# Kernel tuning notes

Hardware: AMD Instinct MI355X
Metric: run time of the kernel (lower is better)

Reference implementation:

```python
import jax, jax.numpy as jnp
import numpy as np

B, NQ, NKV = 8, 256, 1024
DQ, DK, DV = 256, 256, 256
H = 128  # num_hiddens
NEG_INF = -1e20


def setup_inputs() -> dict:
    key = jax.random.key(0)
    k1, k2, k3, k4, k5, k6, k7 = jax.random.split(key, 7)
    s = 0.05
    return {
        "Q_batch": jax.random.normal(k1, (B, NQ, DQ), jnp.float32),
        "K_batch": jax.random.normal(k2, (B, NKV, DK), jnp.float32),
        "V_batch": jax.random.normal(k3, (B, NKV, DV), jnp.float32),
        "valid_lens": jax.random.randint(k4, (B,), 1, NKV, jnp.int32),
        # Learned params (torch nn.Linear stores weight as (out, in); no bias)
        "Wq": jax.random.normal(k5, (H, DQ), jnp.float32) * s,
        "Wk": jax.random.normal(k6, (H, DK), jnp.float32) * s,
        "Wv": jax.random.normal(k7, (H,), jnp.float32) * s,  # W_v: Linear(H -> 1)
    }


def reference(Q_batch, K_batch, V_batch, valid_lens, Wq, Wk, Wv):
    # Project queries and keys to hidden size H
    q = jnp.einsum('bqd,hd->bqh', Q_batch, Wq)            # (B, NQ, H)
    k = jnp.einsum('bkd,hd->bkh', K_batch, Wk)            # (B, NKV, H)
    # Broadcast add -> tanh -> score projection (materializes (B,NQ,NKV,H))
    S = jnp.tanh(q[:, :, None, :] + k[:, None, :, :])     # (B, NQ, NKV, H)
    scores = jnp.einsum('bqkh,h->bqk', S, Wv)             # (B, NQ, NKV)
    # Masked softmax: 'left' => positions >= valid_len are invalid
    kv_idx = jnp.arange(NKV)                              # (NKV,)
    mask = kv_idx[None, None, :] >= valid_lens[:, None, None]  # (B,1,NKV) broadcast over queries
    scores = jnp.where(mask, NEG_INF, scores)
    attn = jax.nn.softmax(scores, axis=-1)                # (B, NQ, NKV)
    # Dropout is identity in eval mode (rate 0.0)
    return jnp.einsum('bqk,bkv->bqv', attn, V_batch)      # (B, NQ, DV)
```

## Files before the change

kernel.cpp:

```cpp
#include <hip/hip_runtime.h>
#include <hip/hip_bf16.h>
#include <math.h>

#define BB   8
#define NQ   256
#define NKV  1024
#define DD   256
#define HH   128
#define KSPLIT 4
#define KCH  256
#define NITEMS (BB * (NQ / 8) * KSPLIT)
#define NWORK  512

typedef float f16v __attribute__((ext_vector_type(16)));

__global__ __launch_bounds__(256) void proj_exp_kernel(
    const float* __restrict__ Q, const float* __restrict__ K,
    const float* __restrict__ Wq, const float* __restrict__ Wk,
    float* __restrict__ eqb, float* __restrict__ ekb)
{
    __shared__ __align__(16) float At[32][20];
    __shared__ __align__(16) float Wt[32][132];

    const int bid = blockIdx.x;
    const bool isQ = bid < (BB * NQ / 16);
    const float* A = isQ ? Q : K;
    const float* W = isQ ? Wq : Wk;
    float* Out     = isQ ? eqb : ekb;
    const int arow0 = (isQ ? bid : bid - (BB * NQ / 16)) * 16;

    const int tid = threadIdx.x;
    const int rc  = tid >> 5;
    const int hc  = tid & 31;

    float4 c0 = {0.f,0.f,0.f,0.f}, c1 = c0;

    float4 a4;
    float4 w4[4];

    if (tid < 128)
        a4 = *(const float4*)(A + (size_t)(arow0 + (tid >> 3)) * DD + (tid & 7) * 4);
#pragma unroll
    for (int t = 0; t < 4; ++t) {
        int idx = tid + t * 256;
        int h = idx >> 3, dw = idx & 7;
        w4[t] = *(const float4*)(W + (size_t)h * DD + dw * 4);
    }

    for (int ch = 0; ch < 8; ++ch) {
        __syncthreads();
        if (tid < 128) {
            int r_st = tid >> 3, dq = tid & 7;
            At[dq*4+0][r_st] = a4.x;
            At[dq*4+1][r_st] = a4.y;
            At[dq*4+2][r_st] = a4.z;
            At[dq*4+3][r_st] = a4.w;
        }
#pragma unroll
        for (int t = 0; t < 4; ++t) {
            int idx = tid + t * 256;
            int h = idx >> 3, dw = idx & 7;
            Wt[dw*4+0][h] = w4[t].x;
            Wt[dw*4+1][h] = w4[t].y;
            Wt[dw*4+2][h] = w4[t].z;
            Wt[dw*4+3][h] = w4[t].w;
        }
        __syncthreads();
        if (ch + 1 < 8) {
            const int dc = (ch + 1) * 32;
            if (tid < 128)
                a4 = *(const float4*)(A + (size_t)(arow0 + (tid >> 3)) * DD + dc + (tid & 7) * 4);
#pragma unroll
            for (int t = 0; t < 4; ++t) {
                int idx = tid + t * 256;
                int h = idx >> 3, dw = idx & 7;
                w4[t] = *(const float4*)(W + (size_t)h * DD + dc + dw * 4);
            }
        }
#pragma unroll
        for (int d = 0; d < 32; ++d) {
            float a0  = At[d][rc];
            float a1  = At[d][rc + 8];
            float4 wv = *(const float4*)&Wt[d][hc * 4];
            c0.x = fmaf(a0, wv.x, c0.x); c0.y = fmaf(a0, wv.y, c0.y);
            c0.z = fmaf(a0, wv.z, c0.z); c0.w = fmaf(a0, wv.w, c0.w);
            c1.x = fmaf(a1, wv.x, c1.x); c1.y = fmaf(a1, wv.y, c1.y);
            c1.z = fmaf(a1, wv.z, c1.z); c1.w = fmaf(a1, wv.w, c1.w);
        }
    }

    float4 o;
    float* p0 = Out + (size_t)(arow0 + rc) * HH + hc * 4;
    o.x = __expf(2.f*c0.x); o.y = __expf(2.f*c0.y);
    o.z = __expf(2.f*c0.z); o.w = __expf(2.f*c0.w);
    *(float4*)p0 = o;
    float* p1 = Out + (size_t)(arow0 + rc + 8) * HH + hc * 4;
    o.x = __expf(2.f*c1.x); o.y = __expf(2.f*c1.y);
    o.z = __expf(2.f*c1.z); o.w = __expf(2.f*c1.w);
    *(float4*)p1 = o;
}

__global__ __launch_bounds__(512) void attn_partial_kernel(
    const float* __restrict__ V, const int* __restrict__ vls,
    const float* __restrict__ Wv,
    const float* __restrict__ eqb, const float* __restrict__ ekb,
    float* __restrict__ pvb, float* __restrict__ mlb,
    unsigned int* __restrict__ qcnt)
{
    __shared__ __align__(16) float sc[8][KCH];
    __shared__ __align__(16) float red[4][8][KCH];
    __shared__ int curs;

    const int tid  = threadIdx.x;
    const int w    = tid >> 6;
    const int lane = tid & 63;
    const int qg = w & 1;
    const int ks = ((w >> 1) << 3) + (lane >> 3);
    const int hg = lane & 7;

    f16v nw2;
    float swv = 0.f;
#pragma unroll
    for (int i = 0; i < 4; ++i) {
        float4 v4 = *(const float4*)(Wv + hg * 16 + i * 4);
        nw2[i*4+0] = -2.f * v4.x; nw2[i*4+1] = -2.f * v4.y;
        nw2[i*4+2] = -2.f * v4.z; nw2[i*4+3] = -2.f * v4.w;
        swv += v4.x + v4.y + v4.z + v4.w;
    }

    for (;;) {
        __syncthreads();
        if (tid == 0) curs = (int)atomicAdd(qcnt, 1u);
        __syncthreads();
        const int idx = curs;
        if (idx >= NITEMS) break;

        const int s  = idx >> 8;
        const int t  = idx & 255;
        const int b  = t >> 5;
        const int k0 = s << 8;
        const int r0 = t * 8;
        const int vl = vls[b];

        if (k0 >= vl) {
            if (tid < 8) {
                mlb[((r0 + tid) * KSPLIT + s) * 2 + 0] = -1e30f;
                mlb[((r0 + tid) * KSPLIT + s) * 2 + 1] = 0.f;
            }
            continue;
        }

        const int kcnt = min(vl - k0, KCH);
        const int nst  = (kcnt + 31) >> 5;

        f16v eqr[4];
#pragma unroll
        for (int r = 0; r < 4; ++r) {
            const float4* p = (const float4*)(eqb + (size_t)(r0 + qg*4 + r) * HH + hg * 16);
            float4 x0 = p[0], x1 = p[1], x2 = p[2], x3 = p[3];
            f16v e;
            e[0]=x0.x;e[1]=x0.y;e[2]=x0.z;e[3]=x0.w; e[4]=x1.x;e[5]=x1.y;e[6]=x1.z;e[7]=x1.w;
            e[8]=x2.x;e[9]=x2.y;e[10]=x2.z;e[11]=x2.w; e[12]=x3.x;e[13]=x3.y;e[14]=x3.z;e[15]=x3.w;
            eqr[r] = e;
        }

        const float* ekbase = ekb + ((size_t)(b * NKV) + k0) * HH + hg * 16;

        auto loadEk = [&](f16v& e, int step) {
            const float4* p = (const float4*)(ekbase + (size_t)(step * 32 + ks) * HH);
            float4 x0 = p[0], x1 = p[1], x2 = p[2], x3 = p[3];
            e[0]=x0.x;e[1]=x0.y;e[2]=x0.z;e[3]=x0.w; e[4]=x1.x;e[5]=x1.y;e[6]=x1.z;e[7]=x1.w;
            e[8]=x2.x;e[9]=x2.y;e[10]=x2.z;e[11]=x2.w; e[12]=x3.x;e[13]=x3.y;e[14]=x3.z;e[15]=x3.w;
        };

        auto body = [&](const f16v& e, int step) {
            float a0 = swv, a1 = swv, a2 = swv, a3 = swv;
#pragma unroll
            for (int j = 0; j < 16; ++j) {
                float ej = e[j];
                float t0 = fmaf(eqr[0][j], ej, 1.0f);
                float t1 = fmaf(eqr[1][j], ej, 1.0f);
                float t2 = fmaf(eqr[2][j], ej, 1.0f);
                float t3 = fmaf(eqr[3][j], ej, 1.0f);
                float r0v = __builtin_amdgcn_rcpf(t0);
                float r1v = __builtin_amdgcn_rcpf(t1);
                float r2v = __builtin_amdgcn_rcpf(t2);
                float r3v = __builtin_amdgcn_rcpf(t3);
                float nj = nw2[j];
                a0 = fmaf(nj, r0v, a0);
                a1 = fmaf(nj, r1v, a1);
                a2 = fmaf(nj, r2v, a2);
                a3 = fmaf(nj, r3v, a3);
            }
            a0 += __shfl_xor(a0, 1); a0 += __shfl_xor(a0, 2); a0 += __shfl_xor(a0, 4);
            a1 += __shfl_xor(a1, 1); a1 += __shfl_xor(a1, 2); a1 += __shfl_xor(a1, 4);
            a2 += __shfl_xor(a2, 1); a2 += __shfl_xor(a2, 2); a2 += __shfl_xor(a2, 4);
            a3 += __shfl_xor(a3, 1); a3 += __shfl_xor(a3, 2); a3 += __shfl_xor(a3, 4);
            if (hg == 0) {
                int kk = step * 32 + ks;
                sc[qg*4+0][kk] = a0;
                sc[qg*4+1][kk] = a1;
                sc[qg*4+2][kk] = a2;
                sc[qg*4+3][kk] = a3;
            }
        };

        f16v ekA, ekB;
        loadEk(ekA, 0);
        for (int st = 0; st < nst; st += 2) {
            if (st + 1 < nst) loadEk(ekB, st + 1);
            body(ekA, st);
            if (st + 1 < nst) {
                if (st + 2 < nst) loadEk(ekA, st + 2);
                body(ekB, st + 1);
            }
        }
        __syncthreads();

        {
            float m = -1e30f;
            float sv[4];
#pragma unroll
            for (int i = 0; i < 4; ++i) {
                int kk = i * 64 + lane;
                float sval = sc[w][kk];
                sv[i] = sval;
                if (k0 + kk < vl) m = fmaxf(m, sval);
            }
#pragma unroll
            for (int off = 1; off < 64; off <<= 1) m = fmaxf(m, __shfl_xor(m, off));
            float sum = 0.f;
#pragma unroll
            for (int i = 0; i < 4; ++i) {
                int kk = i * 64 + lane;
                float p = (k0 + kk < vl) ? __expf(sv[i] - m) : 0.f;
                sum += p;
                sc[w][kk] = p;
            }
#pragma unroll
            for (int off = 1; off < 64; off <<= 1) sum += __shfl_xor(sum, off);
            if (lane == 0) {
                mlb[((r0 + w) * KSPLIT + s) * 2 + 0] = m;
                mlb[((r0 + w) * KSPLIT + s) * 2 + 1] = sum;
            }
        }
        __syncthreads();

        float4 acc[8];
#pragma unroll
        for (int r = 0; r < 8; ++r) acc[r] = make_float4(0.f, 0.f, 0.f, 0.f);
        {
            const int kbase = w * 32;
            if (kbase < kcnt) {
                const float* vb = V + ((size_t)b * NKV + k0 + kbase) * DD + lane * 4;
                for (int kk = 0; kk < 32; kk += 4) {
                    float4 pr[8];
#pragma unroll
                    for (int r = 0; r < 8; ++r)
                        pr[r] = *(const float4*)&sc[r][kbase + kk];
#pragma unroll
                    for (int u = 0; u < 4; ++u) {
                        float4 vv = *(const float4*)(vb + (size_t)(kk + u) * DD);
#pragma unroll
                        for (int r = 0; r < 8; ++r) {
                            float p = (u == 0) ? pr[r].x : (u == 1) ? pr[r].y
                                    : (u == 2) ? pr[r].z : pr[r].w;
                            acc[r].x = fmaf(p, vv.x, acc[r].x);
                            acc[r].y = fmaf(p, vv.y, acc[r].y);
                            acc[r].z = fmaf(p, vv.z, acc[r].z);
                            acc[r].w = fmaf(p, vv.w, acc[r].w);
                        }
                    }
                }
            }
        }
        if (w < 4) {
#pragma unroll
            for (int r = 0; r < 8; ++r)
                *(float4*)&red[w][r][lane * 4] = acc[r];
        }
        __syncthreads();
        if (w >= 4) {
#pragma unroll
            for (int r = 0; r < 8; ++r) {
                float4 tv = *(const float4*)&red[w - 4][r][lane * 4];
                tv.x += acc[r].x; tv.y += acc[r].y;
                tv.z += acc[r].z; tv.w += acc[r].w;
                *(float4*)&red[w - 4][r][lane * 4] = tv;
            }
        }
        __syncthreads();
        {
            float4 o = {0.f, 0.f, 0.f, 0.f};
#pragma unroll
            for (int ss = 0; ss < 4; ++ss) {
                float4 tv = *(const float4*)&red[ss][w][lane * 4];
                o.x += tv.x; o.y += tv.y; o.z += tv.z; o.w += tv.w;
            }
            ((float4*)(pvb + ((size_t)(r0 + w) * KSPLIT + s) * KCH))[lane] = o;
        }
    }
}

__global__ __launch_bounds__(256) void combine_kernel(
    const float* __restrict__ pvb, const float* __restrict__ mlb,
    float* __restrict__ out)
{
    const int tid  = threadIdx.x;
    const int r    = blockIdx.x * 4 + (tid >> 6);
    const int lane = tid & 63;

    float mv[KSPLIT], lv[KSPLIT];
#pragma unroll
    for (int s = 0; s < KSPLIT; ++s) {
        mv[s] = mlb[(r * KSPLIT + s) * 2 + 0];
        lv[s] = mlb[(r * KSPLIT + s) * 2 + 1];
    }
    float M = fmaxf(fmaxf(mv[0], mv[1]), fmaxf(mv[2], mv[3]));
    float coef[KSPLIT];
    float L = 0.f;
#pragma unroll
    for (int s = 0; s < KSPLIT; ++s) {
        coef[s] = __expf(mv[s] - M);
        L = fmaf(lv[s], coef[s], L);
    }
    float rinv = 1.0f / L;

    float4 acc = {0.f, 0.f, 0.f, 0.f};
#pragma unroll
    for (int s = 0; s < KSPLIT; ++s) {
        float4 pv = ((const float4*)(pvb + ((size_t)r * KSPLIT + s) * KCH))[lane];
        float cs = coef[s];
        acc.x = fmaf(cs, pv.x, acc.x);
        acc.y = fmaf(cs, pv.y, acc.y);
        acc.z = fmaf(cs, pv.z, acc.z);
        acc.w = fmaf(cs, pv.w, acc.w);
    }
    acc.x *= rinv; acc.y *= rinv; acc.z *= rinv; acc.w *= rinv;
    *(float4*)(out + (size_t)r * DD + lane * 4) = acc;
}

extern "C" void kernel_launch(void* const* d_in, const int* in_sizes, int n_in,
                              void* d_out, int out_size, void* d_ws, size_t ws_size,
                              hipStream_t stream) {
    const float* Q   = (const float*)d_in[0];
    const float* K   = (const float*)d_in[1];
    const float* V   = (const float*)d_in[2];
    const int*   vls = (const int*)  d_in[3];
    const float* Wq  = (const float*)d_in[4];
    const float* Wk  = (const float*)d_in[5];
    const float* Wv  = (const float*)d_in[6];
    float* out = (float*)d_out;

    float* eq = (float*)d_ws;
    float* ek = eq + (size_t)BB * NQ * HH;
    float* pv = ek + (size_t)BB * NKV * HH;
    float* ml = pv + (size_t)BB * NQ * KSPLIT * KCH;
    unsigned int* qcnt = (unsigned int*)(ml + (size_t)BB * NQ * KSPLIT * 2);

    hipMemsetAsync(qcnt, 0, sizeof(unsigned int), stream);
    proj_exp_kernel<<<(BB*NQ + BB*NKV) / 16, 256, 0, stream>>>(Q, K, Wq, Wk, eq, ek);
    attn_partial_kernel<<<NWORK, 512, 0, stream>>>(V, vls, Wv, eq, ek, pv, ml, qcnt);
    combine_kernel<<<BB * NQ / 4, 256, 0, stream>>>(pv, ml, out);
}
```

Baseline: 144.5 us.

## Drop max-subtraction in softmax, accumulate partials with atomics, finer KV split

Scores come from Wv times a value in (-1,1), so they are bounded and exp can be taken without subtracting the row max. The change exponentiates scores directly, accumulates the row sums and the P·V partials into global buffers with atomicAdd, and replaces the combine kernel with a simple divide. It also halves the KV chunk size and doubles the split count so the work balances better across masked lengths. The cost is many float atomics, a larger memset, and overflow risk if the score magnitudes were ever large.

```diff
diff --git a/kernel.cpp b/kernel.cpp
--- a/kernel.cpp
+++ b/kernel.cpp
@@ -7,8 +7,8 @@
 #define NKV  1024
 #define DD   256
 #define HH   128
-#define KSPLIT 4
-#define KCH  256
+#define KSPLIT 8
+#define KCH  128
 #define NITEMS (BB * (NQ / 8) * KSPLIT)
 #define NWORK  512
 
@@ -104,11 +104,11 @@
     const float* __restrict__ V, const int* __restrict__ vls,
     const float* __restrict__ Wv,
     const float* __restrict__ eqb, const float* __restrict__ ekb,
-    float* __restrict__ pvb, float* __restrict__ mlb,
+    float* __restrict__ acc_out, float* __restrict__ lsum,
     unsigned int* __restrict__ qcnt)
 {
     __shared__ __align__(16) float sc[8][KCH];
-    __shared__ __align__(16) float red[4][8][KCH];
+    __shared__ __align__(16) float red[4][8][DD];
     __shared__ int curs;
 
     const int tid  = threadIdx.x;
@@ -138,17 +138,11 @@
         const int s  = idx >> 8;
         const int t  = idx & 255;
         const int b  = t >> 5;
-        const int k0 = s << 8;
+        const int k0 = s << 7;
         const int r0 = t * 8;
         const int vl = vls[b];
 
-        if (k0 >= vl) {
-            if (tid < 8) {
-                mlb[((r0 + tid) * KSPLIT + s) * 2 + 0] = -1e30f;
-                mlb[((r0 + tid) * KSPLIT + s) * 2 + 1] = 0.f;
-            }
-            continue;
-        }
+        if (k0 >= vl) continue;
 
         const int kcnt = min(vl - k0, KCH);
         const int nst  = (kcnt + 31) >> 5;
@@ -198,10 +192,11 @@
             a3 += __shfl_xor(a3, 1); a3 += __shfl_xor(a3, 2); a3 += __shfl_xor(a3, 4);
             if (hg == 0) {
                 int kk = step * 32 + ks;
-                sc[qg*4+0][kk] = a0;
-                sc[qg*4+1][kk] = a1;
-                sc[qg*4+2][kk] = a2;
-                sc[qg*4+3][kk] = a3;
+                bool valid = (k0 + kk) < vl;
+                sc[qg*4+0][kk] = valid ? __expf(a0) : 0.f;
+                sc[qg*4+1][kk] = valid ? __expf(a1) : 0.f;
+                sc[qg*4+2][kk] = valid ? __expf(a2) : 0.f;
+                sc[qg*4+3][kk] = valid ? __expf(a3) : 0.f;
             }
         };
 
@@ -215,45 +210,32 @@
                 body(ekB, st + 1);
             }
         }
+        if (hg == 0) {
+            for (int st = nst; st < (KCH >> 5); ++st) {
+                int kk = st * 32 + ks;
+                sc[qg*4+0][kk] = 0.f;
+                sc[qg*4+1][kk] = 0.f;
+                sc[qg*4+2][kk] = 0.f;
+                sc[qg*4+3][kk] = 0.f;
+            }
+        }
         __syncthreads();
 
         {
-            float m = -1e30f;
-            float sv[4];
-#pragma unroll
-            for (int i = 0; i < 4; ++i) {
-                int kk = i * 64 + lane;
-                float sval = sc[w][kk];
-                sv[i] = sval;
-                if (k0 + kk < vl) m = fmaxf(m, sval);
-            }
-#pragma unroll
-            for (int off = 1; off < 64; off <<= 1) m = fmaxf(m, __shfl_xor(m, off));
-            float sum = 0.f;
-#pragma unroll
-            for (int i = 0; i < 4; ++i) {
-                int kk = i * 64 + lane;
-                float p = (k0 + kk < vl) ? __expf(sv[i] - m) : 0.f;
-                sum += p;
-                sc[w][kk] = p;
-            }
+            float sum = sc[w][lane] + sc[w][64 + lane];
 #pragma unroll
             for (int off = 1; off < 64; off <<= 1) sum += __shfl_xor(sum, off);
-            if (lane == 0) {
-                mlb[((r0 + w) * KSPLIT + s) * 2 + 0] = m;
-                mlb[((r0 + w) * KSPLIT + s) * 2 + 1] = sum;
-            }
-        }
-        __syncthreads();
+            if (lane == 0) atomicAdd(&lsum[r0 + w], sum);
+        }
 
         float4 acc[8];
 #pragma unroll
         for (int r = 0; r < 8; ++r) acc[r] = make_float4(0.f, 0.f, 0.f, 0.f);
         {
-            const int kbase = w * 32;
+            const int kbase = w * 16;
             if (kbase < kcnt) {
                 const float* vb = V + ((size_t)b * NKV + k0 + kbase) * DD + lane * 4;
-                for (int kk = 0; kk < 32; kk += 4) {
+                for (int kk = 0; kk < 16; kk += 4) {
                     float4 pr[8];
 #pragma unroll
                     for (int r = 0; r < 8; ++r)
@@ -297,47 +279,26 @@
                 float4 tv = *(const float4*)&red[ss][w][lane * 4];
                 o.x += tv.x; o.y += tv.y; o.z += tv.z; o.w += tv.w;
             }
-            ((float4*)(pvb + ((size_t)(r0 + w) * KSPLIT + s) * KCH))[lane] = o;
+            float* dst = acc_out + (size_t)(r0 + w) * DD + lane * 4;
+            atomicAdd(dst + 0, o.x);
+            atomicAdd(dst + 1, o.y);
+            atomicAdd(dst + 2, o.z);
+            atomicAdd(dst + 3, o.w);
         }
     }
 }
 
-__global__ __launch_bounds__(256) void combine_kernel(
-    const float* __restrict__ pvb, const float* __restrict__ mlb,
+__global__ __launch_bounds__(256) void divide_kernel(
+    const float* __restrict__ acc_out, const float* __restrict__ lsum,
     float* __restrict__ out)
 {
-    const int tid  = threadIdx.x;
-    const int r    = blockIdx.x * 4 + (tid >> 6);
-    const int lane = tid & 63;
-
-    float mv[KSPLIT], lv[KSPLIT];
-#pragma unroll
-    for (int s = 0; s < KSPLIT; ++s) {
-        mv[s] = mlb[(r * KSPLIT + s) * 2 + 0];
-        lv[s] = mlb[(r * KSPLIT + s) * 2 + 1];
-    }
-    float M = fmaxf(fmaxf(mv[0], mv[1]), fmaxf(mv[2], mv[3]));
-    float coef[KSPLIT];
-    float L = 0.f;
-#pragma unroll
-    for (int s = 0; s < KSPLIT; ++s) {
-        coef[s] = __expf(mv[s] - M);
-        L = fmaf(lv[s], coef[s], L);
-    }
-    float rinv = 1.0f / L;
-
-    float4 acc = {0.f, 0.f, 0.f, 0.f};
-#pragma unroll
-    for (int s = 0; s < KSPLIT; ++s) {
-        float4 pv = ((const float4*)(pvb + ((size_t)r * KSPLIT + s) * KCH))[lane];
-        float cs = coef[s];
-        acc.x = fmaf(cs, pv.x, acc.x);
-        acc.y = fmaf(cs, pv.y, acc.y);
-        acc.z = fmaf(cs, pv.z, acc.z);
-        acc.w = fmaf(cs, pv.w, acc.w);
-    }
-    acc.x *= rinv; acc.y *= rinv; acc.z *= rinv; acc.w *= rinv;
-    *(float4*)(out + (size_t)r * DD + lane * 4) = acc;
+    const int idx  = blockIdx.x * 256 + threadIdx.x;
+    const int r    = idx >> 6;
+    const int lane = idx & 63;
+    float rinv = 1.0f / lsum[r];
+    float4 a = *(const float4*)(acc_out + (size_t)r * DD + lane * 4);
+    a.x *= rinv; a.y *= rinv; a.z *= rinv; a.w *= rinv;
+    *(float4*)(out + (size_t)r * DD + lane * 4) = a;
 }
 
 extern "C" void kernel_launch(void* const* d_in, const int* in_sizes, int n_in,
@@ -352,14 +313,14 @@
     const float* Wv  = (const float*)d_in[6];
     float* out = (float*)d_out;
 
-    float* eq = (float*)d_ws;
-    float* ek = eq + (size_t)BB * NQ * HH;
-    float* pv = ek + (size_t)BB * NKV * HH;
-    float* ml = pv + (size_t)BB * NQ * KSPLIT * KCH;
-    unsigned int* qcnt = (unsigned int*)(ml + (size_t)BB * NQ * KSPLIT * 2);
-
-    hipMemsetAsync(qcnt, 0, sizeof(unsigned int), stream);
+    float* eq  = (float*)d_ws;
+    float* ek  = eq  + (size_t)BB * NQ * HH;
+    float* acc = ek  + (size_t)BB * NKV * HH;
+    float* ls  = acc + (size_t)BB * NQ * DD;
+    unsigned int* qcnt = (unsigned int*)(ls + (size_t)BB * NQ);
+
+    hipMemsetAsync(acc, 0, ((size_t)BB * NQ * DD + BB * NQ) * sizeof(float) + sizeof(unsigned int), stream);
     proj_exp_kernel<<<(BB*NQ + BB*NKV) / 16, 256, 0, stream>>>(Q, K, Wq, Wk, eq, ek);
-    attn_partial_kernel<<<NWORK, 512, 0, stream>>>(V, vls, Wv, eq, ek, pv, ml, qcnt);
-    combine_kernel<<<BB * NQ / 4, 256, 0, stream>>>(pv, ml, out);
+    attn_partial_kernel<<<NWORK, 512, 0, stream>>>(V, vls, Wv, eq, ek, acc, ls, qcnt);
+    divide_kernel<<<BB * NQ / 4, 256, 0, stream>>>(acc, ls, out);
 }
```

After: 163.6 us. 13.2% more time.
